# Optimization experiments

Measured on AMD Instinct MI355X. Metric: run time of the kernel, lower is better.

Reference implementation:

```python
import jax, jax.numpy as jnp
import numpy as np

B, N, DIM, HEADS, DIM_HEAD = 1, 8192, 512, 8, 64  # dim == heads*dim_head required by pos_emb
EPS = 1e-12  # F.normalize eps


def setup_inputs() -> dict:
    key = jax.random.key(0)
    ks = jax.random.split(key, 13)
    w = lambda k, shape: jax.random.normal(k, shape, dtype=jnp.float32) * 0.02
    return {
        "x_in": jax.random.normal(ks[0], (B, N, DIM), dtype=jnp.float32),
        "task_x": jax.random.normal(ks[1], (B, N, DIM), dtype=jnp.float32),
        "Ges": jax.random.uniform(ks[2], (1, 1, N, N), dtype=jnp.float32) / N,  # OT transport plan (precomputed constant)
        "Wq": w(ks[3], (DIM, DIM)),
        "Wk": w(ks[4], (DIM, DIM)),
        "Wv": w(ks[5], (DIM, DIM)),
        "rescale": jnp.ones((HEADS, 1, 1), dtype=jnp.float32),
        "Wp": w(ks[6], (DIM, DIM)),
        "bp": jnp.zeros((DIM,), dtype=jnp.float32),
        "W1": w(ks[7], (DIM, DIM)),
        "b1": jnp.zeros((DIM,), dtype=jnp.float32),
        "W2": w(ks[8], (DIM, DIM)),
        "b2": jnp.zeros((DIM,), dtype=jnp.float32),
    }


def _l2norm(x):
    # F.normalize(p=2, dim=-1): x / max(||x||, eps)
    n = jnp.sqrt(jnp.sum(x * x, axis=-1, keepdims=True))
    return x / jnp.maximum(n, EPS)


def reference(x_in, task_x, Ges, Wq, Wk, Wv, rescale, Wp, bp, W1, b1, W2, b2):
    b, n, c = x_in.shape
    q_inp = x_in @ Wq.T          # [b,n,hd]
    k_inp = x_in @ Wk.T
    v_inp = x_in @ Wv.T
    split = lambda t: t.reshape(b, n, HEADS, DIM_HEAD).transpose(0, 2, 1, 3)  # [b,h,n,d]
    q, k, v, tx = split(q_inp), split(k_inp), split(v_inp), split(task_x)
    guided = (Ges @ tx) * v       # [b,h,n,d]: OT-guided embedding multiply
    # channel attention: operate along n, attend over d
    qT = _l2norm(q.transpose(0, 1, 3, 2))   # [b,h,d,n]
    kT = _l2norm(k.transpose(0, 1, 3, 2))   # [b,h,d,n]
    gT = guided.transpose(0, 1, 3, 2)        # [b,h,d,n]
    attn = jnp.einsum('bhdn,bhen->bhde', kT, qT) * rescale  # [b,h,d,d]
    attn = jax.nn.softmax(attn, axis=-1)
    x = attn @ gT                 # [b,h,d,n]
    x = x.transpose(0, 3, 1, 2).reshape(b, n, HEADS * DIM_HEAD)  # [b,n,hd]
    out_c = x @ Wp.T + bp
    out_p = (jax.nn.gelu(v_inp @ W1.T + b1, approximate=False)) @ W2.T + b2
    return out_c + out_p
```

## Files before the change

### kernel.cpp

```cpp
#include <hip/hip_runtime.h>
#include <hip/hip_bf16.h>

typedef unsigned short u16;
typedef __attribute__((ext_vector_type(8))) short short8v;
typedef __attribute__((ext_vector_type(4))) float f32x4;

typedef __attribute__((address_space(3))) char lds_char;
typedef const __attribute__((address_space(1))) char g_char;

__device__ __forceinline__ u16 f2bf(float f) {
    union { float f; unsigned int u; } x; x.f = f;
    unsigned int u = x.u;
    return (u16)((u + 0x7FFFu + ((u >> 16) & 1u)) >> 16);
}
__device__ __forceinline__ float bf2f(u16 h) {
    union { unsigned int u; float f; } x; x.u = ((unsigned int)h) << 16;
    return x.f;
}
__device__ __forceinline__ u16 cvtbf(float f) {
    return __builtin_bit_cast(u16, __float2bfloat16(f));
}
__device__ __forceinline__ void gload16(const void* g, void* l) {
    __builtin_amdgcn_global_load_lds((g_char*)g, (lds_char*)l, 16, 0, 0);
}

template<int EPI>
__global__ __launch_bounds__(256, 2) void gemm_256(
    const u16* __restrict__ Ab, int lda,
    const u16* __restrict__ Bt, int ldb,
    void* __restrict__ Cp, int ldc, int K)
{
    __shared__ alignas(16) char smem[49152];

    const int t     = threadIdx.x;
    const int lane  = t & 63;
    const int wid   = t >> 6;
    const int m0    = blockIdx.x * 256;
    const int n0    = blockIdx.y * 128;
    const int kbase = blockIdx.z * K;
    const int wr    = wid >> 1, wc = wid & 1;
    const int lr    = lane & 15, q4 = lane >> 4;

    f32x4 acc[8][4];
    #pragma unroll
    for (int i = 0; i < 8; ++i)
        #pragma unroll
        for (int j = 0; j < 4; ++j)
            acc[i][j] = (f32x4){0.f, 0.f, 0.f, 0.f};

    const int nsteps = K >> 6;
    for (int kt = 0; kt < nsteps; ++kt) {
        const int k0 = kbase + (kt << 6);
        #pragma unroll
        for (int p = 0; p < 8; ++p) {
            int o   = p * 4096 + t * 16;
            int row = o >> 7;
            int cb  = (o & 127) ^ ((row & 7) << 4);
            gload16(Ab + (size_t)(m0 + row) * (size_t)lda + k0 + (cb >> 1),
                    smem + o);
        }
        #pragma unroll
        for (int p = 0; p < 4; ++p) {
            int o   = p * 4096 + t * 16;
            int row = o >> 7;
            int cb  = (o & 127) ^ ((row & 7) << 4);
            gload16(Bt + (size_t)(n0 + row) * (size_t)ldb + k0 + (cb >> 1),
                    smem + 32768 + o);
        }
        __syncthreads();

        #pragma unroll
        for (int kh = 0; kh < 2; ++kh) {
            short8v a[8], b[4];
            #pragma unroll
            for (int i = 0; i < 8; ++i) {
                int ar = wr * 128 + i * 16 + lr;
                a[i] = *(const short8v*)(smem + ar * 128 +
                        ((kh * 64 + q4 * 16) ^ ((ar & 7) << 4)));
            }
            #pragma unroll
            for (int i = 0; i < 4; ++i) {
                int br = wc * 64 + i * 16 + lr;
                b[i] = *(const short8v*)(smem + 32768 + br * 128 +
                        ((kh * 64 + q4 * 16) ^ ((br & 7) << 4)));
            }
            #pragma unroll
            for (int mi = 0; mi < 8; ++mi)
                #pragma unroll
                for (int ni = 0; ni < 4; ++ni)
                    acc[mi][ni] = __builtin_amdgcn_mfma_f32_16x16x32_bf16(
                        a[mi], b[ni], acc[mi][ni], 0, 0, 0);
        }
        __syncthreads();
    }

    const size_t zoff = (size_t)blockIdx.z * 8192ull * (size_t)ldc;
    #pragma unroll
    for (int mi = 0; mi < 8; ++mi) {
        #pragma unroll
        for (int ni = 0; ni < 4; ++ni) {
            const int gc = n0 + wc * 64 + ni * 16 + lr;
            #pragma unroll
            for (int j = 0; j < 4; ++j) {
                const int gr = m0 + wr * 128 + mi * 16 + q4 * 4 + j;
                float v = acc[mi][ni][j];
                if constexpr (EPI == 0) {
                    ((u16*)Cp)[(size_t)gr * ldc + gc] = f2bf(v);
                } else {
                    ((float*)Cp)[zoff + (size_t)gr * ldc + gc] = v;
                }
            }
        }
    }
}

template<int EPI>
__global__ __launch_bounds__(256, 4) void gemm_k(
    const u16* __restrict__ Ab, int lda,
    const u16* __restrict__ Bt, int ldb,
    void* __restrict__ Cp, int ldc, int K)
{
    __shared__ alignas(16) char smem[32768];

    const int t     = threadIdx.x;
    const int lane  = t & 63;
    const int wid   = t >> 6;
    const int m0    = blockIdx.x * 128;
    const int n0    = blockIdx.y * 128;
    const int kbase = blockIdx.z * K;
    const int wr    = wid >> 1, wc = wid & 1;
    const int lr    = lane & 15, q4 = lane >> 4;

    f32x4 acc[4][4];
    #pragma unroll
    for (int i = 0; i < 4; ++i)
        #pragma unroll
        for (int j = 0; j < 4; ++j)
            acc[i][j] = (f32x4){0.f, 0.f, 0.f, 0.f};

    const int nsteps = K >> 6;
    for (int kt = 0; kt < nsteps; ++kt) {
        const int k0 = kbase + (kt << 6);
        #pragma unroll
        for (int p = 0; p < 4; ++p) {
            int o   = p * 4096 + t * 16;
            int row = o >> 7;
            int cb  = (o & 127) ^ ((row & 7) << 4);
            gload16(Ab + (size_t)(m0 + row) * (size_t)lda + k0 + (cb >> 1),
                    smem + o);
        }
        #pragma unroll
        for (int p = 0; p < 4; ++p) {
            int o   = p * 4096 + t * 16;
            int row = o >> 7;
            int cb  = (o & 127) ^ ((row & 7) << 4);
            gload16(Bt + (size_t)(n0 + row) * (size_t)ldb + k0 + (cb >> 1),
                    smem + 16384 + o);
        }
        __syncthreads();

        #pragma unroll
        for (int kh = 0; kh < 2; ++kh) {
            short8v a[4], b[4];
            #pragma unroll
            for (int i = 0; i < 4; ++i) {
                int ar = wr * 64 + i * 16 + lr;
                a[i] = *(const short8v*)(smem + ar * 128 +
                        ((kh * 64 + q4 * 16) ^ ((ar & 7) << 4)));
            }
            #pragma unroll
            for (int i = 0; i < 4; ++i) {
                int br = wc * 64 + i * 16 + lr;
                b[i] = *(const short8v*)(smem + 16384 + br * 128 +
                        ((kh * 64 + q4 * 16) ^ ((br & 7) << 4)));
            }
            #pragma unroll
            for (int mi = 0; mi < 4; ++mi)
                #pragma unroll
                for (int ni = 0; ni < 4; ++ni)
                    acc[mi][ni] = __builtin_amdgcn_mfma_f32_16x16x32_bf16(
                        a[mi], b[ni], acc[mi][ni], 0, 0, 0);
        }
        __syncthreads();
    }

    const size_t zoff = (size_t)blockIdx.z * 8192ull * (size_t)ldc;
    #pragma unroll
    for (int mi = 0; mi < 4; ++mi) {
        #pragma unroll
        for (int ni = 0; ni < 4; ++ni) {
            const int gc = n0 + wc * 64 + ni * 16 + lr;
            #pragma unroll
            for (int j = 0; j < 4; ++j) {
                const int gr = m0 + wr * 64 + mi * 16 + q4 * 4 + j;
                float v = acc[mi][ni][j];
                if constexpr (EPI == 0) {
                    ((u16*)Cp)[(size_t)gr * ldc + gc] = f2bf(v);
                } else {
                    ((float*)Cp)[zoff + (size_t)gr * ldc + gc] = v;
                }
            }
        }
    }
}

template<int KZ, int MODE>
__global__ void k_cmb(const float* __restrict__ P, const u16* __restrict__ QKV,
                      const float* __restrict__ bvec, void* __restrict__ dst)
{
    for (int i = blockIdx.x * 256 + threadIdx.x; i < 1048576;
         i += gridDim.x * 256) {
        const int r = i >> 7, c = (i & 127) * 4;
        f32x4 s = ((const f32x4*)P)[i];
        #pragma unroll
        for (int z = 1; z < KZ; ++z) {
            f32x4 q = ((const f32x4*)P)[(size_t)z * 1048576 + i];
            s[0] += q[0]; s[1] += q[1]; s[2] += q[2]; s[3] += q[3];
        }
        if constexpr (MODE == 1) {
            ushort4 v = *(const ushort4*)(QKV + (size_t)r * 1536 + 1024 + c);
            ushort4 o;
            o.x = cvtbf(s[0] * bf2f(v.x)); o.y = cvtbf(s[1] * bf2f(v.y));
            o.z = cvtbf(s[2] * bf2f(v.z)); o.w = cvtbf(s[3] * bf2f(v.w));
            *(ushort4*)((u16*)dst + (size_t)r * 1024 + c) = o;
        } else if constexpr (MODE == 2) {
            float4 b = *(const float4*)(bvec + c);
            float x0 = s[0] + b.x, x1 = s[1] + b.y, x2 = s[2] + b.z, x3 = s[3] + b.w;
            ushort4 o;
            o.x = cvtbf(0.5f * x0 * (1.0f + erff(x0 * 0.70710678118f)));
            o.y = cvtbf(0.5f * x1 * (1.0f + erff(x1 * 0.70710678118f)));
            o.z = cvtbf(0.5f * x2 * (1.0f + erff(x2 * 0.70710678118f)));
            o.w = cvtbf(0.5f * x3 * (1.0f + erff(x3 * 0.70710678118f)));
            *(ushort4*)((u16*)dst + (size_t)r * 1024 + 512 + c) = o;
        } else {
            float4 b = *(const float4*)(bvec + c);
            float4 o = {s[0] + b.x, s[1] + b.y, s[2] + b.z, s[3] + b.w};
            *(float4*)((float*)dst + (size_t)r * 512 + c) = o;
        }
    }
}

__global__ void k_cges(const float* __restrict__ g, u16* __restrict__ gb)
{
    const int total = 8388608;
    for (int i = blockIdx.x * 256 + threadIdx.x; i < total;
         i += gridDim.x * 256) {
        const float4* s = (const float4*)(g + (size_t)i * 8);
        float4 a = s[0], b = s[1];
        uint4 o;
        o.x = (unsigned)cvtbf(a.x) | ((unsigned)cvtbf(a.y) << 16);
        o.y = (unsigned)cvtbf(a.z) | ((unsigned)cvtbf(a.w) << 16);
        o.z = (unsigned)cvtbf(b.x) | ((unsigned)cvtbf(b.y) << 16);
        o.w = (unsigned)cvtbf(b.z) | ((unsigned)cvtbf(b.w) << 16);
        *(uint4*)(gb + (size_t)i * 8) = o;
    }
}

__global__ void k_convert(const float* __restrict__ x_in,
                          const float* __restrict__ Wq, const float* __restrict__ Wk,
                          const float* __restrict__ Wv, const float* __restrict__ W1,
                          u16* __restrict__ XB, u16* __restrict__ WqkvB,
                          u16* __restrict__ W1B)
{
    const int C1 = 1048576;
    const int C2 = 196608;
    const int C3 = 65536;
    for (int i = blockIdx.x * blockDim.x + threadIdx.x; i < C1 + C2 + C3;
         i += gridDim.x * blockDim.x) {
        const float* src; u16* dst;
        if (i < C1) { src = x_in + (size_t)i * 4; dst = XB + (size_t)i * 4; }
        else if (i < C1 + C2) {
            int e = (i - C1) * 4;
            if (e < 262144)      src = Wq + e;
            else if (e < 524288) src = Wk + (e - 262144);
            else                 src = Wv + (e - 524288);
            dst = WqkvB + e;
        } else {
            int e = (i - C1 - C2) * 4;
            src = W1 + e; dst = W1B + e;
        }
        float4 v = *reinterpret_cast<const float4*>(src);
        ushort4 h;
        h.x = f2bf(v.x); h.y = f2bf(v.y); h.z = f2bf(v.z); h.w = f2bf(v.w);
        *reinterpret_cast<ushort4*>(dst) = h;
    }
}

__global__ void k_transpose(const float* __restrict__ tx, u16* __restrict__ txt)
{
    __shared__ float tile[64][65];
    const int n0 = blockIdx.x * 64;
    const int c0 = blockIdx.y * 64;
    const int t = threadIdx.x;
    #pragma unroll
    for (int p = 0; p < 4; ++p) {
        int q = p * 256 + t;
        int r = q >> 4, s = q & 15;
        float4 v = *reinterpret_cast<const float4*>(tx + (size_t)(n0 + r) * 512 + c0 + s * 4);
        tile[r][s * 4 + 0] = v.x; tile[r][s * 4 + 1] = v.y;
        tile[r][s * 4 + 2] = v.z; tile[r][s * 4 + 3] = v.w;
    }
    __syncthreads();
    #pragma unroll
    for (int p = 0; p < 4; ++p) {
        int q = p * 256 + t;
        int cc = q >> 4, s = q & 15;
        ushort4 h;
        h.x = f2bf(tile[s * 4 + 0][cc]); h.y = f2bf(tile[s * 4 + 1][cc]);
        h.z = f2bf(tile[s * 4 + 2][cc]); h.w = f2bf(tile[s * 4 + 3][cc]);
        *reinterpret_cast<ushort4*>(txt + (size_t)(c0 + cc) * 8192 + n0 + s * 4) = h;
    }
}

__global__ void k_colsq(const u16* __restrict__ QKV, float* __restrict__ colsq)
{
    const int t = threadIdx.x;
    const int c8 = t & 127, rs = t >> 7;
    float a[8];
    #pragma unroll
    for (int j = 0; j < 8; ++j) a[j] = 0.f;
    const int row0 = blockIdx.x * 64;
    for (int rr = rs; rr < 64; rr += 2) {
        uint4 u = *reinterpret_cast<const uint4*>(QKV + (size_t)(row0 + rr) * 1536 + c8 * 8);
        unsigned int w[4] = {u.x, u.y, u.z, u.w};
        #pragma unroll
        for (int q = 0; q < 4; ++q) {
            float f0 = bf2f((u16)(w[q] & 0xffffu));
            float f1 = bf2f((u16)(w[q] >> 16));
            a[2 * q]     += f0 * f0;
            a[2 * q + 1] += f1 * f1;
        }
    }
    #pragma unroll
    for (int j = 0; j < 8; ++j) atomicAdd(&colsq[c8 * 8 + j], a[j]);
}

__global__ void k_gram(const u16* __restrict__ QKV, float* __restrict__ Sb)
{
    __shared__ u16 Qt[4][64];
    __shared__ u16 Kt[4][64];
    const int h = blockIdx.x >> 6;
    const int chunk = blockIdx.x & 63;
    const int t = threadIdx.x;
    const int e = t & 63;
    const int dg = t >> 6;
    float acc[16];
    #pragma unroll
    for (int k = 0; k < 16; ++k) acc[k] = 0.f;
    const int rowbase = chunk * 128;
    for (int p = 0; p < 32; ++p) {
        __syncthreads();
        if (t < 64) {
            const int mat = t >> 5, sub = t & 31, r = sub >> 3, seg = sub & 7;
            const int row = rowbase + p * 4 + r;
            const int col = (mat ? 512 : 0) + h * 64 + seg * 8;
            uint4 v = *reinterpret_cast<const uint4*>(QKV + (size_t)row * 1536 + col);
            u16* dst = mat ? &Kt[r][seg * 8] : &Qt[r][seg * 8];
            *reinterpret_cast<uint4*>(dst) = v;
        }
        __syncthreads();
        #pragma unroll
        for (int r = 0; r < 4; ++r) {
            const float q = bf2f(Qt[r][e]);
            short8v kv0 = *reinterpret_cast<const short8v*>(&Kt[r][dg * 16]);
            short8v kv1 = *reinterpret_cast<const short8v*>(&Kt[r][dg * 16 + 8]);
            #pragma unroll
            for (int k = 0; k < 8; ++k) {
                acc[k]     += bf2f((u16)kv0[k]) * q;
                acc[k + 8] += bf2f((u16)kv1[k]) * q;
            }
        }
    }
    #pragma unroll
    for (int k = 0; k < 16; ++k)
        atomicAdd(&Sb[h * 4096 + (dg * 16 + k) * 64 + e], acc[k]);
}

__global__ void k_softmax(const float* __restrict__ Sb, const float* __restrict__ colsq,
                          const float* __restrict__ rescale, float* __restrict__ Abuf)
{
    const int h = blockIdx.x;
    const int t = threadIdx.x;
    const float rsc = rescale[h];
    const float nq = fmaxf(sqrtf(colsq[h * 64 + t]), 1e-12f);
    for (int d = 0; d < 64; ++d) {
        const float nk = fmaxf(sqrtf(colsq[512 + h * 64 + d]), 1e-12f);
        float v = Sb[h * 4096 + d * 64 + t] / (nk * nq) * rsc;
        float m = v;
        #pragma unroll
        for (int off = 32; off > 0; off >>= 1) m = fmaxf(m, __shfl_xor(m, off, 64));
        float p = expf(v - m);
        float s = p;
        #pragma unroll
        for (int off = 32; off > 0; off >>= 1) s += __shfl_xor(s, off, 64);
        Abuf[h * 4096 + d * 64 + t] = p / s;
    }
}

__global__ void k_buildbt(const float* __restrict__ Abuf, const float* __restrict__ Wp,
                          const float* __restrict__ W2, const float* __restrict__ bp,
                          const float* __restrict__ b2, u16* __restrict__ BtC,
                          float* __restrict__ bsum)
{
    const int g = blockIdx.x * 256 + threadIdx.x;
    const int j = g >> 10, c = g & 1023;
    if (c < 512) {
        const int h = c >> 6, e = c & 63;
        const float* Ah = Abuf + h * 4096 + e;
        const float* Wph = Wp + (size_t)j * 512 + h * 64;
        float s = 0.f;
        #pragma unroll 8
        for (int d = 0; d < 64; ++d) s += Ah[d * 64] * Wph[d];
        BtC[(size_t)j * 1024 + c] = f2bf(s);
        if (c == 0) bsum[j] = bp[j] + b2[j];
    } else {
        BtC[(size_t)j * 1024 + c] = f2bf(W2[(size_t)j * 512 + (c - 512)]);
    }
}

extern "C" void kernel_launch(void* const* d_in, const int* in_sizes, int n_in,
                              void* d_out, int out_size, void* d_ws, size_t ws_size,
                              hipStream_t stream)
{
    const float* x_in    = (const float*)d_in[0];
    const float* task_x  = (const float*)d_in[1];
    const float* Ges     = (const float*)d_in[2];
    const float* Wq      = (const float*)d_in[3];
    const float* Wk      = (const float*)d_in[4];
    const float* Wv      = (const float*)d_in[5];
    const float* rescale = (const float*)d_in[6];
    const float* Wp      = (const float*)d_in[7];
    const float* bp      = (const float*)d_in[8];
    const float* W1      = (const float*)d_in[9];
    const float* b1      = (const float*)d_in[10];
    const float* W2      = (const float*)d_in[11];
    const float* b2      = (const float*)d_in[12];
    float* out = (float*)d_out;
    char* ws = (char*)d_ws;

    u16*   XB    = (u16*)  (ws + 0);
    u16*   TXT   = (u16*)  (ws + 8388608);
    u16*   QKV   = (u16*)  (ws + 16777216);
    u16*   AH    = (u16*)  (ws + 41943040);
    u16*   WqkvB = (u16*)  (ws + 58720256);
    u16*   W1B   = (u16*)  (ws + 60293120);
    u16*   BtC   = (u16*)  (ws + 60817408);
    float* colsq = (float*)(ws + 61865984);
    float* Sb    = (float*)(ws + 61870080);
    float* Abuf  = (float*)(ws + 62001152);
    float* bsum  = (float*)(ws + 62132224);
    float* P     = (float*)(ws + 62134272);
    u16*   GesB  = (u16*)  (ws + 129243136);
    (void)in_sizes; (void)n_in; (void)out_size; (void)ws_size;

    hipMemsetAsync(colsq, 0, 135168, stream);

    k_convert  <<<2048, 256, 0, stream>>>(x_in, Wq, Wk, Wv, W1, XB, WqkvB, W1B);
    k_transpose<<<dim3(128, 8), 256, 0, stream>>>(task_x, TXT);
    k_cges     <<<2048, 256, 0, stream>>>(Ges, GesB);

    gemm_256<0><<<dim3(32, 12, 1), 256, 0, stream>>>(
        XB, 512, WqkvB, 512, QKV, 1536, 512);

    k_colsq  <<<128, 256, 0, stream>>>(QKV, colsq);
    k_gram   <<<512, 256, 0, stream>>>(QKV, Sb);
    k_softmax<<<8, 64, 0, stream>>>(Sb, colsq, rescale, Abuf);
    k_buildbt<<<2048, 256, 0, stream>>>(Abuf, Wp, W2, bp, b2, BtC, bsum);

    gemm_256<4><<<dim3(32, 4, 4), 256, 0, stream>>>(
        GesB, 8192, TXT, 8192, P, 512, 2048);
    k_cmb<4, 1><<<1024, 256, 0, stream>>>(P, QKV, nullptr, AH);

    gemm_k<4><<<dim3(64, 4, 2), 256, 0, stream>>>(
        QKV + 1024, 1536, W1B, 512, P, 512, 256);
    k_cmb<2, 2><<<1024, 256, 0, stream>>>(P, nullptr, b1, AH);

    gemm_k<4><<<dim3(64, 4, 2), 256, 0, stream>>>(
        AH, 1024, BtC, 1024, P, 512, 512);
    k_cmb<2, 3><<<1024, 256, 0, stream>>>(P, nullptr, bsum, out);
}
```

Baseline: 407.0 us.

## Fuse Ges fp32-to-bf16 conversion into guided GEMM, drop separate cast pass

Removes the standalone kernel that converted the 8192x8192 Ges matrix to bf16. A new register-only MFMA GEMM loads fp32 Ges directly, converts it in registers, and multiplies against transposed task_x with split-K of 4 and double-buffered global loads. This avoids writing and re-reading a 128MB bf16 copy. In exchange the GEMM reads fp32 A with no LDS staging, and each wave reloads A rows that other waves also load.

```diff
diff --git a/kernel.cpp b/kernel.cpp
--- a/kernel.cpp
+++ b/kernel.cpp
@@ -22,6 +22,99 @@
 }
 __device__ __forceinline__ void gload16(const void* g, void* l) {
     __builtin_amdgcn_global_load_lds((g_char*)g, (lds_char*)l, 16, 0, 0);
+}
+
+template<int SPLITK>
+__global__ __launch_bounds__(512, 2) void gemm_guided(
+    const float* __restrict__ Ges,
+    const u16* __restrict__ TXT,
+    float* __restrict__ P)
+{
+    const int t    = threadIdx.x;
+    const int lane = t & 63;
+    const int wid  = t >> 6;
+    const int m0   = blockIdx.x * 64;
+    const int n0   = wid * 64;
+    const int kz   = 8192 / SPLITK;
+    const int kbase = blockIdx.y * kz;
+    const int lr   = lane & 15, q4 = lane >> 4;
+
+    f32x4 acc[4][4];
+    #pragma unroll
+    for (int i = 0; i < 4; ++i)
+        #pragma unroll
+        for (int j = 0; j < 4; ++j)
+            acc[i][j] = (f32x4){0.f, 0.f, 0.f, 0.f};
+
+    const float* Ab[4];
+    const u16*  Bb[4];
+    #pragma unroll
+    for (int mi = 0; mi < 4; ++mi)
+        Ab[mi] = Ges + (size_t)(m0 + mi * 16 + lr) * 8192 + kbase + q4 * 8;
+    #pragma unroll
+    for (int ni = 0; ni < 4; ++ni)
+        Bb[ni] = TXT + (size_t)(n0 + ni * 16 + lr) * 8192 + kbase + q4 * 8;
+
+    float4 a0[4][2], a1[4][2];
+    uint4  b0[4],  b1[4];
+
+    auto LOAD = [&](float4 (&af)[4][2], uint4 (&bf)[4], int kt) {
+        const int ko = kt << 5;
+        #pragma unroll
+        for (int mi = 0; mi < 4; ++mi) {
+            af[mi][0] = *(const float4*)(Ab[mi] + ko);
+            af[mi][1] = *(const float4*)(Ab[mi] + ko + 4);
+        }
+        #pragma unroll
+        for (int ni = 0; ni < 4; ++ni)
+            bf[ni] = *(const uint4*)(Bb[ni] + ko);
+    };
+    auto COMP = [&](float4 (&af)[4][2], uint4 (&bf)[4]) {
+        short8v a[4];
+        #pragma unroll
+        for (int mi = 0; mi < 4; ++mi) {
+            short8v v;
+            #pragma unroll
+            for (int j = 0; j < 4; ++j) {
+                v[j]     = (short)cvtbf(af[mi][0][j]);
+                v[j + 4] = (short)cvtbf(af[mi][1][j]);
+            }
+            a[mi] = v;
+        }
+        #pragma unroll
+        for (int mi = 0; mi < 4; ++mi)
+            #pragma unroll
+            for (int ni = 0; ni < 4; ++ni)
+                acc[mi][ni] = __builtin_amdgcn_mfma_f32_16x16x32_bf16(
+                    a[mi], __builtin_bit_cast(short8v, bf[ni]), acc[mi][ni], 0, 0, 0);
+    };
+
+    const int nsteps = kz >> 5;
+    LOAD(a0, b0, 0);
+    int kt = 0;
+    for (; kt + 2 < nsteps; kt += 2) {
+        LOAD(a1, b1, kt + 1);
+        COMP(a0, b0);
+        LOAD(a0, b0, kt + 2);
+        COMP(a1, b1);
+    }
+    LOAD(a1, b1, kt + 1);
+    COMP(a0, b0);
+    COMP(a1, b1);
+
+    float* Pz = P + (size_t)blockIdx.y * 8192ull * 512ull;
+    #pragma unroll
+    for (int mi = 0; mi < 4; ++mi) {
+        #pragma unroll
+        for (int ni = 0; ni < 4; ++ni) {
+            const int gc = n0 + ni * 16 + lr;
+            #pragma unroll
+            for (int j = 0; j < 4; ++j) {
+                const int gr = m0 + mi * 16 + q4 * 4 + j;
+                Pz[(size_t)gr * 512 + gc] = acc[mi][ni][j];
+            }
+        }
+    }
 }
 
 template<int EPI>
@@ -240,22 +333,6 @@
     }
 }
 
-__global__ void k_cges(const float* __restrict__ g, u16* __restrict__ gb)
-{
-    const int total = 8388608;
-    for (int i = blockIdx.x * 256 + threadIdx.x; i < total;
-         i += gridDim.x * 256) {
-        const float4* s = (const float4*)(g + (size_t)i * 8);
-        float4 a = s[0], b = s[1];
-        uint4 o;
-        o.x = (unsigned)cvtbf(a.x) | ((unsigned)cvtbf(a.y) << 16);
-        o.y = (unsigned)cvtbf(a.z) | ((unsigned)cvtbf(a.w) << 16);
-        o.z = (unsigned)cvtbf(b.x) | ((unsigned)cvtbf(b.y) << 16);
-        o.w = (unsigned)cvtbf(b.z) | ((unsigned)cvtbf(b.w) << 16);
-        *(uint4*)(gb + (size_t)i * 8) = o;
-    }
-}
-
 __global__ void k_convert(const float* __restrict__ x_in,
                           const float* __restrict__ Wq, const float* __restrict__ Wk,
                           const float* __restrict__ Wv, const float* __restrict__ W1,
@@ -450,14 +527,12 @@
     float* Abuf  = (float*)(ws + 62001152);
     float* bsum  = (float*)(ws + 62132224);
     float* P     = (float*)(ws + 62134272);
-    u16*   GesB  = (u16*)  (ws + 129243136);
     (void)in_sizes; (void)n_in; (void)out_size; (void)ws_size;
 
     hipMemsetAsync(colsq, 0, 135168, stream);
 
     k_convert  <<<2048, 256, 0, stream>>>(x_in, Wq, Wk, Wv, W1, XB, WqkvB, W1B);
     k_transpose<<<dim3(128, 8), 256, 0, stream>>>(task_x, TXT);
-    k_cges     <<<2048, 256, 0, stream>>>(Ges, GesB);
 
     gemm_256<0><<<dim3(32, 12, 1), 256, 0, stream>>>(
         XB, 512, WqkvB, 512, QKV, 1536, 512);
@@ -467,8 +542,7 @@
     k_softmax<<<8, 64, 0, stream>>>(Sb, colsq, rescale, Abuf);
     k_buildbt<<<2048, 256, 0, stream>>>(Abuf, Wp, W2, bp, b2, BtC, bsum);
 
-    gemm_256<4><<<dim3(32, 4, 4), 256, 0, stream>>>(
-        GesB, 8192, TXT, 8192, P, 512, 2048);
+    gemm_guided<4><<<dim3(128, 4), 512, 0, stream>>>(Ges, TXT, P);
     k_cmb<4, 1><<<1024, 256, 0, stream>>>(P, QKV, nullptr, AH);
 
     gemm_k<4><<<dim3(64, 4, 2), 256, 0, stream>>>(
```

Result: slower. 598.8 us (+47.1%).
